# Optimization experiments

Hardware: AMD Instinct MI355X
Metric: run time of the kernel (lower is better)

The kernel has to match this reference:

```python
import jax, jax.numpy as jnp
import numpy as np

DIM = 1024
NUM_HEADS = 16
HEAD_DIM = DIM // NUM_HEADS
SCALE = HEAD_DIM ** -0.5


def rotate_half(x):
    x1, x2 = jnp.split(x, 2, axis=-1)
    return jnp.concatenate((-x2, x1), axis=-1)


def setup_inputs() -> dict:
    key = jax.random.key(0)
    ks = jax.random.split(key, 8)
    B, N = 2, 2048
    x = jax.random.normal(ks[0], (B, N, DIM), dtype=jnp.float32)
    # RoPE tables, broadcast over batch and heads
    pos = jnp.arange(N, dtype=jnp.float32)[:, None]
    inv_freq = 1.0 / (10000.0 ** (jnp.arange(0, HEAD_DIM, 2, dtype=jnp.float32) / HEAD_DIM))
    ang = pos * inv_freq[None, :]                       # [N, HEAD_DIM/2]
    ang = jnp.concatenate([ang, ang], axis=-1)          # [N, HEAD_DIM]
    rope_cos = jnp.cos(ang)[None, None]                 # [1,1,N,HEAD_DIM]
    rope_sin = jnp.sin(ang)[None, None]
    s = DIM ** -0.5
    qkv_w = jax.random.normal(ks[1], (3 * DIM, DIM), dtype=jnp.float32) * s
    qkv_b = jnp.zeros((3 * DIM,), dtype=jnp.float32)
    proj_w = jax.random.normal(ks[2], (DIM, DIM), dtype=jnp.float32) * s
    proj_b = jnp.zeros((DIM,), dtype=jnp.float32)
    return {"x": x, "rope_cos": rope_cos, "rope_sin": rope_sin,
            "qkv_w": qkv_w, "qkv_b": qkv_b, "proj_w": proj_w, "proj_b": proj_b}


def reference(x, rope_cos, rope_sin, qkv_w, qkv_b, proj_w, proj_b):
    B, N, C = x.shape
    H, D = NUM_HEADS, HEAD_DIM
    qkv = x @ qkv_w.T + qkv_b                            # [B,N,3C]
    qkv = qkv.reshape(B, N, 3, H, D).transpose(2, 0, 3, 1, 4)  # [3,B,H,N,D]
    q, k, v = qkv[0], qkv[1], qkv[2]
    # RoPE on q, k
    q = q * rope_cos + rotate_half(q) * rope_sin
    k = k * rope_cos + rotate_half(k) * rope_sin
    # scaled dot-product attention
    scores = jnp.einsum('bhnd,bhmd->bhnm', q, k) * SCALE
    attn = jax.nn.softmax(scores, axis=-1)
    out = jnp.einsum('bhnm,bhmd->bhnd', attn, v)         # [B,H,N,D]
    out = out.transpose(0, 2, 1, 3).reshape(B, N, C)
    return out @ proj_w.T + proj_b
```

## Files before the change

kernel.cpp:

```cpp
#include <hip/hip_runtime.h>
#include <hip/hip_bf16.h>

#define NUM_HEADS 16
#define HEAD_DIM 64
#define DIM 1024
#define NTOK 2048
#define MTOT 4096

typedef __attribute__((ext_vector_type(8))) short bf16x8;
typedef __attribute__((ext_vector_type(4))) float f32x4;

__device__ __forceinline__ unsigned short f2bf(float f) {
    union { __hip_bfloat16 h; unsigned short u; } c;
    c.h = __float2bfloat16(f);
    return c.u;
}

__device__ __forceinline__ void gload16(const unsigned short* g, unsigned short* l) {
    __builtin_amdgcn_global_load_lds(
        (const __attribute__((address_space(1))) void*)g,
        (__attribute__((address_space(3))) void*)l, 16, 0, 0);
}

__global__ __launch_bounds__(256) void k_conv3(
    const float* __restrict__ s0, unsigned short* __restrict__ d0, int n0,
    const float* __restrict__ s1, unsigned short* __restrict__ d1, int n1,
    const float* __restrict__ s2, unsigned short* __restrict__ d2, int n2)
{
    int blk = blockIdx.x;
    int b0 = n0 >> 11, b1 = n1 >> 11;
    const float* s; unsigned short* d; int i;
    if (blk < b0)            { s = s0; d = d0; i = blk; }
    else if (blk < b0 + b1)  { s = s1; d = d1; i = blk - b0; }
    else                     { s = s2; d = d2; i = blk - b0 - b1; }
    int idx = (i * 256 + threadIdx.x) * 8;
    float4 a = *(const float4*)(s + idx);
    float4 b = *(const float4*)(s + idx + 4);
    union { unsigned short us[8]; uint4 u4; } p;
    p.us[0] = f2bf(a.x); p.us[1] = f2bf(a.y); p.us[2] = f2bf(a.z); p.us[3] = f2bf(a.w);
    p.us[4] = f2bf(b.x); p.us[5] = f2bf(b.y); p.us[6] = f2bf(b.z); p.us[7] = f2bf(b.w);
    *(uint4*)(d + idx) = p.u4;
}

__global__ __launch_bounds__(256) void k_gemm_qkv(
    const unsigned short* __restrict__ xb, const unsigned short* __restrict__ wb,
    const float* __restrict__ bias, const float* __restrict__ rcos,
    const float* __restrict__ rsin,
    unsigned short* __restrict__ qb, unsigned short* __restrict__ kb,
    unsigned short* __restrict__ vtb)
{
    __shared__ __align__(16) unsigned char smem[34816];
    unsigned short* As = (unsigned short*)smem;
    unsigned short* Bs = (unsigned short*)(smem + 16384);

    const int tid  = threadIdx.x;
    const int lane = tid & 63;
    const int wid  = tid >> 6;
    const int lr   = lane & 15;
    const int g    = lane >> 4;
    const int wm   = (wid >> 1) * 64;
    const int wn   = (wid & 1) * 64;
    const int m0   = blockIdx.x * 128;
    const int n0   = blockIdx.y * 128;

    f32x4 acc[4][4];
    #pragma unroll
    for (int i = 0; i < 4; ++i)
        #pragma unroll
        for (int j = 0; j < 4; ++j) acc[i][j] = (f32x4){0.f, 0.f, 0.f, 0.f};

    for (int k0 = 0; k0 < DIM; k0 += 64) {
        #pragma unroll
        for (int it = 0; it < 4; ++it) {
            int p   = tid + it * 256;
            int row = p >> 3;
            int c   = (p & 7) ^ (row & 7);
            gload16(xb + (size_t)(m0 + row) * DIM + k0 + c*8, As + p*8);
            gload16(wb + (size_t)(n0 + row) * DIM + k0 + c*8, Bs + p*8);
        }
        __syncthreads();
        #pragma unroll
        for (int kk = 0; kk < 2; ++kk) {
            bf16x8 af[4], bfr[4];
            #pragma unroll
            for (int i = 0; i < 4; ++i) {
                int row = wm + i*16 + lr;
                af[i] = *(const bf16x8*)(As + row*64 + (((kk*4 + g) ^ (row & 7)) << 3));
            }
            #pragma unroll
            for (int j = 0; j < 4; ++j) {
                int row = wn + j*16 + lr;
                bfr[j] = *(const bf16x8*)(Bs + row*64 + (((kk*4 + g) ^ (row & 7)) << 3));
            }
            #pragma unroll
            for (int i = 0; i < 4; ++i)
                #pragma unroll
                for (int j = 0; j < 4; ++j)
                    acc[i][j] = __builtin_amdgcn_mfma_f32_16x16x32_bf16(af[i], bfr[j], acc[i][j], 0, 0, 0);
        }
        __syncthreads();
    }

    const int sect = n0 >> 10;
    float bq[4];
    #pragma unroll
    for (int j = 0; j < 4; ++j) bq[j] = bias[n0 + wn + j*16 + lr];

    if (sect < 2) {
        unsigned short* dst = sect ? kb : qb;
        const float sc = sect ? 1.0f : 0.125f * 1.44269504088896f;
        const int h = ((n0 & 1023) + wn) >> 6;
        #pragma unroll
        for (int i = 0; i < 4; ++i) {
            #pragma unroll
            for (int v = 0; v < 4; ++v) {
                int gm = m0 + wm + i*16 + g*4 + v;
                int b  = gm >> 11, n = gm & 2047;
                size_t base = ((size_t)(b*NUM_HEADS + h) * NTOK + n) << 6;
                #pragma unroll
                for (int j = 0; j < 4; ++j) {
                    int d = j*16 + lr;
                    float val = acc[i][j][v] + bq[j];
                    float vp  = acc[i][j^2][v] + bq[j^2];
                    float rot = (j < 2) ? -vp : vp;
                    float c = rcos[n*64 + d], s = rsin[n*64 + d];
                    dst[base + d] = f2bf((val * c + rot * s) * sc);
                }
            }
        }
    } else {
        unsigned short (*vt)[136] = (unsigned short (*)[136])smem;
        __syncthreads();
        #pragma unroll
        for (int i = 0; i < 4; ++i)
            #pragma unroll
            for (int j = 0; j < 4; ++j)
                #pragma unroll
                for (int v = 0; v < 4; ++v) {
                    int row = wm + i*16 + g*4 + v;
                    int c   = wn + j*16 + lr;
                    vt[c][row] = f2bf(acc[i][j][v] + bq[j]);
                }
        __syncthreads();
        const int b = m0 >> 11;
        const int nbase = m0 & 2047;
        #pragma unroll
        for (int it = 0; it < 8; ++it) {
            int c   = (tid >> 4) + it * 16;
            int sc2 = (n0 & 1023) + c;
            int hh  = sc2 >> 6, d = sc2 & 63;
            int nloc = (tid & 15) * 8;
            uint4 val = *(uint4*)&vt[c][nloc];
            *(uint4*)(vtb + ((size_t)(b*NUM_HEADS + hh) * HEAD_DIM + d) * NTOK + nbase + nloc) = val;
        }
    }
}

__global__ __launch_bounds__(256, 4) void k_attn(
    const unsigned short* __restrict__ qb, const unsigned short* __restrict__ kb,
    const unsigned short* __restrict__ vtb, unsigned short* __restrict__ attnb)
{
    __shared__ __align__(16) char sb[40960];

    const int tid  = threadIdx.x;
    const int lane = tid & 63;
    const int w    = tid >> 6;
    const int g    = lane >> 4;
    const int lr   = lane & 15;
    const int q0   = blockIdx.x * 64;
    const int bh   = blockIdx.y;
    const int b    = bh >> 4, h = bh & 15;

    int kfoff[2][4], vfoff[2][4];
    #pragma unroll
    for (int kk = 0; kk < 2; ++kk)
        #pragma unroll
        for (int fn = 0; fn < 4; ++fn) {
            int row = fn*16 + lr;
            int sw  = ((kk*4 + g) ^ (row & 7)) << 4;
            kfoff[kk][fn] = row*128 + sw;
            vfoff[kk][fn] = 16384 + row*128 + sw;
        }
    const int pswz = (lr & 7) << 1;
    int pwoff[4], proff[2];
    #pragma unroll
    for (int fn = 0; fn < 4; ++fn)
        pwoff[fn] = 32768 + w*2048 + lr*128 + (((fn*4 + g) ^ pswz) << 3);
    #pragma unroll
    for (int kk = 0; kk < 2; ++kk)
        proff[kk] = 32768 + w*2048 + lr*128 + (((kk*8 + g*2) ^ pswz) << 3);

    const unsigned short* gk[2];
    const unsigned short* gv[2];
    char* dk[2]; char* dv[2];
    {
        const unsigned short* kbase = kb  + (size_t)bh * NTOK * 64;
        const unsigned short* vbase = vtb + (size_t)bh * HEAD_DIM * NTOK;
        #pragma unroll
        for (int hp = 0; hp < 2; ++hp) {
            int p   = tid + hp * 256;
            int row = p >> 3;
            int c   = (p & 7) ^ (row & 7);
            gk[hp] = kbase + row*64 + c*8;
            gv[hp] = vbase + (size_t)row*NTOK + c*8;
            dk[hp] = sb + p*16;
            dv[hp] = sb + 16384 + p*16;
        }
    }

    bf16x8 qa[2];
    {
        size_t qrow = ((size_t)bh * NTOK + q0 + w*16 + lr) * 64;
        #pragma unroll
        for (int kk = 0; kk < 2; ++kk)
            qa[kk] = *(const bf16x8*)(qb + qrow + kk*32 + g*8);
    }

    const f32x4 z4 = {0.f, 0.f, 0.f, 0.f};
    bf16x8 onesa;
    #pragma unroll
    for (int j = 0; j < 8; ++j) onesa[j] = (short)0x3F80;

    f32x4 o2[4];
    f32x4 ol = z4;
    float m_ = -1e30f;
    #pragma unroll
    for (int fd = 0; fd < 4; ++fd) o2[fd] = z4;

    #pragma unroll
    for (int hp = 0; hp < 2; ++hp) {
        gload16(gk[hp], (unsigned short*)dk[hp]);
        gload16(gv[hp], (unsigned short*)dv[hp]);
        gk[hp] += 4096; gv[hp] += 64;
    }
    __syncthreads();

#define ATTN_ITER(X, DO_STAGE)                                                   \
    {                                                                            \
        if (DO_STAGE) {                                                          \
            _Pragma("unroll")                                                    \
            for (int hp = 0; hp < 2; ++hp) {                                     \
                gload16(gk[hp], (unsigned short*)(dk[hp] + ((X) ^ 8192)));       \
                gload16(gv[hp], (unsigned short*)(dv[hp] + ((X) ^ 8192)));       \
                gk[hp] += 4096; gv[hp] += 64;                                    \
            }                                                                    \
        }                                                                        \
        f32x4 s_[4];                                                             \
        __builtin_amdgcn_s_setprio(1);                                           \
        _Pragma("unroll")                                                        \
        for (int fn = 0; fn < 4; ++fn) {                                         \
            bf16x8 kf = *(const bf16x8*)(sb + kfoff[0][fn] + (X));               \
            s_[fn] = __builtin_amdgcn_mfma_f32_16x16x32_bf16(kf, qa[0], z4, 0, 0, 0); \
        }                                                                        \
        _Pragma("unroll")                                                        \
        for (int fn = 0; fn < 4; ++fn) {                                         \
            bf16x8 kf = *(const bf16x8*)(sb + kfoff[1][fn] + (X));               \
            s_[fn] = __builtin_amdgcn_mfma_f32_16x16x32_bf16(kf, qa[1], s_[fn], 0, 0, 0); \
        }                                                                        \
        __builtin_amdgcn_s_setprio(0);                                           \
        float mmA = fmaxf(fmaxf(s_[0][0], s_[0][1]), fmaxf(s_[0][2], s_[0][3])); \
        float mmB = fmaxf(fmaxf(s_[1][0], s_[1][1]), fmaxf(s_[1][2], s_[1][3])); \
        float mmC = fmaxf(fmaxf(s_[2][0], s_[2][1]), fmaxf(s_[2][2], s_[2][3])); \
        float mmD = fmaxf(fmaxf(s_[3][0], s_[3][1]), fmaxf(s_[3][2], s_[3][3])); \
        float lmax = fmaxf(fmaxf(mmA, mmB), fmaxf(mmC, mmD));                    \
        if (__any(lmax > m_ + 8.f)) {                                            \
            float mx = fmaxf(lmax, __shfl_xor(lmax, 16));                        \
            mx = fmaxf(mx, __shfl_xor(mx, 32));                                  \
            float mn  = fmaxf(m_, mx);                                           \
            float scl = __builtin_amdgcn_exp2f(m_ - mn);                         \
            m_ = mn;                                                             \
            _Pragma("unroll")                                                    \
            for (int v = 0; v < 4; ++v) ol[v] *= scl;                            \
            _Pragma("unroll")                                                    \
            for (int fd = 0; fd < 4; ++fd)                                       \
                _Pragma("unroll")                                                \
                for (int v = 0; v < 4; ++v) o2[fd][v] *= scl;                    \
        }                                                                        \
        _Pragma("unroll")                                                        \
        for (int fn = 0; fn < 4; ++fn) {                                         \
            union { unsigned short us[4]; uint2 u2; } pk4;                       \
            _Pragma("unroll")                                                    \
            for (int v = 0; v < 4; ++v)                                          \
                pk4.us[v] = f2bf(__builtin_amdgcn_exp2f(s_[fn][v] - m_));        \
            *(uint2*)(sb + pwoff[fn]) = pk4.u2;                                  \
        }                                                                        \
        _Pragma("unroll")                                                        \
        for (int kk = 0; kk < 2; ++kk) {                                         \
            bf16x8 pb = *(const bf16x8*)(sb + proff[kk]);                        \
            bf16x8 vf[4];                                                        \
            _Pragma("unroll")                                                    \
            for (int fd = 0; fd < 4; ++fd)                                       \
                vf[fd] = *(const bf16x8*)(sb + vfoff[kk][fd] + (X));             \
            __builtin_amdgcn_s_setprio(1);                                       \
            ol = __builtin_amdgcn_mfma_f32_16x16x32_bf16(onesa, pb, ol, 0, 0, 0); \
            _Pragma("unroll")                                                    \
            for (int fd = 0; fd < 4; ++fd)                                       \
                o2[fd] = __builtin_amdgcn_mfma_f32_16x16x32_bf16(vf[fd], pb, o2[fd], 0, 0, 0); \
            __builtin_amdgcn_s_setprio(0);                                       \
        }                                                                        \
        __syncthreads();                                                         \
    }

    #pragma unroll 1
    for (int t = 0; t < NTOK/64; t += 2) {
        ATTN_ITER(0,    true);
        ATTN_ITER(8192, (t + 2 < NTOK/64));
    }
#undef ATTN_ITER

    const float inv = 1.0f / ol[0];
    const size_t obase = ((size_t)(b*NTOK + q0 + w*16 + lr)) * DIM + h*HEAD_DIM + g*4;
    #pragma unroll
    for (int fd = 0; fd < 4; ++fd) {
        union { unsigned short us[4]; uint2 u2; } pk4;
        #pragma unroll
        for (int v = 0; v < 4; ++v) pk4.us[v] = f2bf(o2[fd][v] * inv);
        *(uint2*)(attnb + obase + fd*16) = pk4.u2;
    }
}

__global__ __launch_bounds__(256) void k_proj(
    const unsigned short* __restrict__ a, const unsigned short* __restrict__ wb,
    const float* __restrict__ bias, float* __restrict__ out)
{
    __shared__ __align__(16) unsigned short As[8192];
    __shared__ __align__(16) unsigned short Bs[8192];

    const int tid  = threadIdx.x;
    const int lane = tid & 63;
    const int wid  = tid >> 6;
    const int lr   = lane & 15;
    const int g    = lane >> 4;
    const int wm   = (wid >> 1) * 64;
    const int wn   = (wid & 1) * 64;
    const int m0   = blockIdx.x * 128;
    const int n0   = blockIdx.y * 128;

    f32x4 acc[4][4];
    #pragma unroll
    for (int i = 0; i < 4; ++i)
        #pragma unroll
        for (int j = 0; j < 4; ++j) acc[i][j] = (f32x4){0.f, 0.f, 0.f, 0.f};

    for (int k0 = 0; k0 < DIM; k0 += 64) {
        #pragma unroll
        for (int it = 0; it < 4; ++it) {
            int p   = tid + it * 256;
            int row = p >> 3;
            int c   = (p & 7) ^ (row & 7);
            gload16(a  + (size_t)(m0 + row) * DIM + k0 + c*8, As + p*8);
            gload16(wb + (size_t)(n0 + row) * DIM + k0 + c*8, Bs + p*8);
        }
        __syncthreads();
        #pragma unroll
        for (int kk = 0; kk < 2; ++kk) {
            bf16x8 af[4], bfr[4];
            #pragma unroll
            for (int i = 0; i < 4; ++i) {
                int row = wm + i*16 + lr;
                af[i] = *(const bf16x8*)(As + row*64 + (((kk*4 + g) ^ (row & 7)) << 3));
            }
            #pragma unroll
            for (int j = 0; j < 4; ++j) {
                int row = wn + j*16 + lr;
                bfr[j] = *(const bf16x8*)(Bs + row*64 + (((kk*4 + g) ^ (row & 7)) << 3));
            }
            #pragma unroll
            for (int i = 0; i < 4; ++i)
                #pragma unroll
                for (int j = 0; j < 4; ++j)
                    acc[i][j] = __builtin_amdgcn_mfma_f32_16x16x32_bf16(af[i], bfr[j], acc[i][j], 0, 0, 0);
        }
        __syncthreads();
    }

    #pragma unroll
    for (int i = 0; i < 4; ++i)
        #pragma unroll
        for (int j = 0; j < 4; ++j)
            #pragma unroll
            for (int v = 0; v < 4; ++v) {
                int row = m0 + wm + i*16 + g*4 + v;
                int col = n0 + wn + j*16 + lr;
                out[(size_t)row * DIM + col] = acc[i][j][v] + bias[col];
            }
}

extern "C" void kernel_launch(void* const* d_in, const int* in_sizes, int n_in,
                              void* d_out, int out_size, void* d_ws, size_t ws_size,
                              hipStream_t stream)
{
    const float* x      = (const float*)d_in[0];
    const float* rcos   = (const float*)d_in[1];
    const float* rsin   = (const float*)d_in[2];
    const float* qkv_w  = (const float*)d_in[3];
    const float* qkv_b  = (const float*)d_in[4];
    const float* proj_w = (const float*)d_in[5];
    const float* proj_b = (const float*)d_in[6];
    float* out = (float*)d_out;

    const size_t BUF = (size_t)2 * NUM_HEADS * NTOK * HEAD_DIM;
    unsigned short* qb    = (unsigned short*)d_ws;
    unsigned short* kb    = qb + BUF;
    unsigned short* vtb   = kb + BUF;
    unsigned short* attnb = vtb + BUF;
    unsigned short* xbf   = attnb + BUF;
    unsigned short* wqkvb = xbf + (size_t)MTOT * DIM;
    unsigned short* wprjb = wqkvb + (size_t)3 * DIM * DIM;

    const int n0 = MTOT * DIM, n1 = 3 * DIM * DIM, n2 = DIM * DIM;
    k_conv3<<<dim3((n0 + n1 + n2) / 2048), 256, 0, stream>>>(
        x, xbf, n0, qkv_w, wqkvb, n1, proj_w, wprjb, n2);

    k_gemm_qkv<<<dim3(32, 24), 256, 0, stream>>>(xbf, wqkvb, qkv_b, rcos, rsin, qb, kb, vtb);
    k_attn<<<dim3(NTOK/64, 32), 256, 0, stream>>>(qb, kb, vtb, attnb);
    k_proj<<<dim3(32, 8), 256, 0, stream>>>(attnb, wprjb, proj_b, out);
}
```

Baseline: 127.9 us.

## Use 32x32 MFMA with register-resident P in attention; retile projection GEMM

The attention kernel now uses 32x32x16 MFMA tiles with 128 queries per block. The probability matrix stays in registers, rearranged via permlane32 swaps instead of being written to and read back from LDS. The row sum is computed with VALU adds rather than an extra MFMA against a ones vector. The projection GEMM tile shrinks to 128x64, doubling the grid for better CU occupancy. The risks are more register pressure (launch bound lowered to 2 blocks/SM), half as many attention blocks, and extra VALU reduction work.

Result: faster. 121.5 us (-5.0%).

```diff
diff --git a/kernel.cpp b/kernel.cpp
--- a/kernel.cpp
+++ b/kernel.cpp
@@ -9,11 +9,33 @@
 
 typedef __attribute__((ext_vector_type(8))) short bf16x8;
 typedef __attribute__((ext_vector_type(4))) float f32x4;
+typedef __attribute__((ext_vector_type(16))) float f32x16;
+typedef __attribute__((ext_vector_type(2))) unsigned int uint2v;
 
 __device__ __forceinline__ unsigned short f2bf(float f) {
     union { __hip_bfloat16 h; unsigned short u; } c;
     c.h = __float2bfloat16(f);
     return c.u;
+}
+
+__device__ __forceinline__ unsigned int packbf(float lo, float hi) {
+    union { unsigned short us[2]; unsigned int u; } p;
+    p.us[0] = f2bf(lo); p.us[1] = f2bf(hi);
+    return p.u;
+}
+
+__device__ __forceinline__ void plswap(unsigned int &a, unsigned int &b) {
+#if __has_builtin(__builtin_amdgcn_permlane32_swap)
+    uint2v r = __builtin_amdgcn_permlane32_swap(a, b, false, false);
+    a = r[0]; b = r[1];
+#else
+    unsigned int pa = (unsigned int)__shfl_xor((int)a, 32);
+    unsigned int pb = (unsigned int)__shfl_xor((int)b, 32);
+    bool hi = (threadIdx.x & 32) != 0;
+    unsigned int an = hi ? pb : a;
+    unsigned int bn = hi ? b : pa;
+    a = an; b = bn;
+#endif
 }
 
 __device__ __forceinline__ void gload16(const unsigned short* g, unsigned short* l) {
@@ -156,39 +178,30 @@
     }
 }
 
-__global__ __launch_bounds__(256, 4) void k_attn(
+__global__ __launch_bounds__(256, 2) void k_attn(
     const unsigned short* __restrict__ qb, const unsigned short* __restrict__ kb,
     const unsigned short* __restrict__ vtb, unsigned short* __restrict__ attnb)
 {
-    __shared__ __align__(16) char sb[40960];
+    __shared__ __align__(16) char sb[32768];
 
     const int tid  = threadIdx.x;
     const int lane = tid & 63;
     const int w    = tid >> 6;
-    const int g    = lane >> 4;
-    const int lr   = lane & 15;
-    const int q0   = blockIdx.x * 64;
+    const int hi   = lane >> 5;
+    const int lc   = lane & 31;
+    const int q0   = blockIdx.x * 128;
     const int bh   = blockIdx.y;
     const int b    = bh >> 4, h = bh & 15;
 
     int kfoff[2][4], vfoff[2][4];
     #pragma unroll
-    for (int kk = 0; kk < 2; ++kk)
-        #pragma unroll
-        for (int fn = 0; fn < 4; ++fn) {
-            int row = fn*16 + lr;
-            int sw  = ((kk*4 + g) ^ (row & 7)) << 4;
-            kfoff[kk][fn] = row*128 + sw;
-            vfoff[kk][fn] = 16384 + row*128 + sw;
-        }
-    const int pswz = (lr & 7) << 1;
-    int pwoff[4], proff[2];
-    #pragma unroll
-    for (int fn = 0; fn < 4; ++fn)
-        pwoff[fn] = 32768 + w*2048 + lr*128 + (((fn*4 + g) ^ pswz) << 3);
-    #pragma unroll
-    for (int kk = 0; kk < 2; ++kk)
-        proff[kk] = 32768 + w*2048 + lr*128 + (((kk*8 + g*2) ^ pswz) << 3);
+    for (int s = 0; s < 2; ++s)
+        #pragma unroll
+        for (int ks = 0; ks < 4; ++ks) {
+            int row = 32*s + lc;
+            kfoff[s][ks] = row*128 + (((2*ks + hi) ^ (row & 7)) << 4);
+            vfoff[s][ks] = 16384 + row*128 + (((2*ks + hi) ^ (row & 7)) << 4);
+        }
 
     const unsigned short* gk[2];
     const unsigned short* gv[2];
@@ -208,24 +221,18 @@
         }
     }
 
-    bf16x8 qa[2];
+    bf16x8 qa[4];
     {
-        size_t qrow = ((size_t)bh * NTOK + q0 + w*16 + lr) * 64;
-        #pragma unroll
-        for (int kk = 0; kk < 2; ++kk)
-            qa[kk] = *(const bf16x8*)(qb + qrow + kk*32 + g*8);
-    }
-
-    const f32x4 z4 = {0.f, 0.f, 0.f, 0.f};
-    bf16x8 onesa;
-    #pragma unroll
-    for (int j = 0; j < 8; ++j) onesa[j] = (short)0x3F80;
-
-    f32x4 o2[4];
-    f32x4 ol = z4;
-    float m_ = -1e30f;
-    #pragma unroll
-    for (int fd = 0; fd < 4; ++fd) o2[fd] = z4;
+        size_t qrow = ((size_t)bh * NTOK + q0 + w*32 + lc) * 64;
+        #pragma unroll
+        for (int ks = 0; ks < 4; ++ks)
+            qa[ks] = *(const bf16x8*)(qb + qrow + ks*16 + hi*8);
+    }
+
+    const f32x16 z16 = {0.f,0.f,0.f,0.f, 0.f,0.f,0.f,0.f, 0.f,0.f,0.f,0.f, 0.f,0.f,0.f,0.f};
+    f32x16 o2[2];
+    o2[0] = z16; o2[1] = z16;
+    float m_ = -1e30f, lsum = 0.f;
 
     #pragma unroll
     for (int hp = 0; hp < 2; ++hp) {
@@ -245,78 +252,108 @@
                 gk[hp] += 4096; gv[hp] += 64;                                    \
             }                                                                    \
         }                                                                        \
-        f32x4 s_[4];                                                             \
-        __builtin_amdgcn_s_setprio(1);                                           \
-        _Pragma("unroll")                                                        \
-        for (int fn = 0; fn < 4; ++fn) {                                         \
-            bf16x8 kf = *(const bf16x8*)(sb + kfoff[0][fn] + (X));               \
-            s_[fn] = __builtin_amdgcn_mfma_f32_16x16x32_bf16(kf, qa[0], z4, 0, 0, 0); \
-        }                                                                        \
-        _Pragma("unroll")                                                        \
-        for (int fn = 0; fn < 4; ++fn) {                                         \
-            bf16x8 kf = *(const bf16x8*)(sb + kfoff[1][fn] + (X));               \
-            s_[fn] = __builtin_amdgcn_mfma_f32_16x16x32_bf16(kf, qa[1], s_[fn], 0, 0, 0); \
-        }                                                                        \
-        __builtin_amdgcn_s_setprio(0);                                           \
-        float mmA = fmaxf(fmaxf(s_[0][0], s_[0][1]), fmaxf(s_[0][2], s_[0][3])); \
-        float mmB = fmaxf(fmaxf(s_[1][0], s_[1][1]), fmaxf(s_[1][2], s_[1][3])); \
-        float mmC = fmaxf(fmaxf(s_[2][0], s_[2][1]), fmaxf(s_[2][2], s_[2][3])); \
-        float mmD = fmaxf(fmaxf(s_[3][0], s_[3][1]), fmaxf(s_[3][2], s_[3][3])); \
-        float lmax = fmaxf(fmaxf(mmA, mmB), fmaxf(mmC, mmD));                    \
+                                          \
+        f32x16 S0, S1;                                                           \
+        {                                                                        \
+            bf16x8 kf0[4], kf1[4];                                               \
+            _Pragma("unroll")                                                    \
+            for (int ks = 0; ks < 4; ++ks) {                                     \
+                kf0[ks] = *(const bf16x8*)(sb + kfoff[0][ks] + (X));             \
+                kf1[ks] = *(const bf16x8*)(sb + kfoff[1][ks] + (X));             \
+            }                                                                    \
+            __builtin_amdgcn_s_setprio(1);                                       \
+            S0 = __builtin_amdgcn_mfma_f32_32x32x16_bf16(kf0[0], qa[0], z16, 0, 0, 0); \
+            S1 = __builtin_amdgcn_mfma_f32_32x32x16_bf16(kf1[0], qa[0], z16, 0, 0, 0); \
+            _Pragma("unroll")                                                    \
+            for (int ks = 1; ks < 4; ++ks) {                                     \
+                S0 = __builtin_amdgcn_mfma_f32_32x32x16_bf16(kf0[ks], qa[ks], S0, 0, 0, 0); \
+                S1 = __builtin_amdgcn_mfma_f32_32x32x16_bf16(kf1[ks], qa[ks], S1, 0, 0, 0); \
+            }                                                                    \
+            __builtin_amdgcn_s_setprio(0);                                       \
+        }                                                                        \
+                          \
+        float t[16];                                                             \
+        _Pragma("unroll")                                                        \
+        for (int r = 0; r < 16; ++r) t[r] = fmaxf(S0[r], S1[r]);                 \
+        _Pragma("unroll")                                                        \
+        for (int st = 8; st > 0; st >>= 1)                                       \
+            _Pragma("unroll")                                                    \
+            for (int i = 0; i < 8; ++i) if (i < st) t[i] = fmaxf(t[i], t[i + st]); \
+        float lmax = t[0];                                                       \
         if (__any(lmax > m_ + 8.f)) {                                            \
-            float mx = fmaxf(lmax, __shfl_xor(lmax, 16));                        \
-            mx = fmaxf(mx, __shfl_xor(mx, 32));                                  \
-            float mn  = fmaxf(m_, mx);                                           \
+            float mx = fmaxf(lmax, __shfl_xor(lmax, 32));                        \
+            float mn = fmaxf(m_, mx);                                            \
             float scl = __builtin_amdgcn_exp2f(m_ - mn);                         \
             m_ = mn;                                                             \
+            lsum *= scl;                                                         \
+            o2[0] *= scl; o2[1] *= scl;                                          \
+        }                                                                        \
+                                               \
+        _Pragma("unroll")                                                        \
+        for (int r = 0; r < 16; ++r) {                                           \
+            S0[r] = __builtin_amdgcn_exp2f(S0[r] - m_);                          \
+            S1[r] = __builtin_amdgcn_exp2f(S1[r] - m_);                          \
+        }                                                                        \
+        _Pragma("unroll")                                                        \
+        for (int r = 0; r < 16; ++r) t[r] = S0[r] + S1[r];                       \
+        _Pragma("unroll")                                                        \
+        for (int st = 8; st > 0; st >>= 1)                                       \
             _Pragma("unroll")                                                    \
-            for (int v = 0; v < 4; ++v) ol[v] *= scl;                            \
-            _Pragma("unroll")                                                    \
-            for (int fd = 0; fd < 4; ++fd)                                       \
-                _Pragma("unroll")                                                \
-                for (int v = 0; v < 4; ++v) o2[fd][v] *= scl;                    \
-        }                                                                        \
-        _Pragma("unroll")                                                        \
-        for (int fn = 0; fn < 4; ++fn) {                                         \
-            union { unsigned short us[4]; uint2 u2; } pk4;                       \
-            _Pragma("unroll")                                                    \
-            for (int v = 0; v < 4; ++v)                                          \
-                pk4.us[v] = f2bf(__builtin_amdgcn_exp2f(s_[fn][v] - m_));        \
-            *(uint2*)(sb + pwoff[fn]) = pk4.u2;                                  \
-        }                                                                        \
-        _Pragma("unroll")                                                        \
-        for (int kk = 0; kk < 2; ++kk) {                                         \
-            bf16x8 pb = *(const bf16x8*)(sb + proff[kk]);                        \
-            bf16x8 vf[4];                                                        \
-            _Pragma("unroll")                                                    \
-            for (int fd = 0; fd < 4; ++fd)                                       \
-                vf[fd] = *(const bf16x8*)(sb + vfoff[kk][fd] + (X));             \
+            for (int i = 0; i < 8; ++i) if (i < st) t[i] += t[i + st];           \
+        lsum += t[0];                                                            \
+                \
+        unsigned int dwA[2][4], dwB[2][4];                                       \
+        _Pragma("unroll")                                                        \
+        for (int c = 0; c < 4; ++c) {                                            \
+            dwA[0][c] = packbf(S0[4*c],     S0[4*c + 1]);                        \
+            dwB[0][c] = packbf(S0[4*c + 2], S0[4*c + 3]);                        \
+            dwA[1][c] = packbf(S1[4*c],     S1[4*c + 1]);                        \
+            dwB[1][c] = packbf(S1[4*c + 2], S1[4*c + 3]);                        \
+        }                                                                        \
+        bf16x8 pB[4];                                                            \
+        _Pragma("unroll")                                                        \
+        for (int t16 = 0; t16 < 4; ++t16) {                                      \
+            int s = t16 >> 1, u = t16 & 1;                                       \
+            unsigned int a0 = dwA[s][2*u], b0 = dwA[s][2*u + 1];                 \
+            unsigned int a1 = dwB[s][2*u], b1 = dwB[s][2*u + 1];                 \
+            plswap(a0, b0);                                                      \
+            plswap(a1, b1);                                                      \
+            union { unsigned int u4[4]; bf16x8 v; } pk;                          \
+            pk.u4[0] = a0; pk.u4[1] = a1; pk.u4[2] = b0; pk.u4[3] = b1;          \
+            pB[t16] = pk.v;                                                      \
+        }                                                                        \
+                             \
+        _Pragma("unroll")                                                        \
+        for (int t16 = 0; t16 < 4; ++t16) {                                      \
+            bf16x8 vf0 = *(const bf16x8*)(sb + vfoff[0][t16] + (X));             \
+            bf16x8 vf1 = *(const bf16x8*)(sb + vfoff[1][t16] + (X));             \
             __builtin_amdgcn_s_setprio(1);                                       \
-            ol = __builtin_amdgcn_mfma_f32_16x16x32_bf16(onesa, pb, ol, 0, 0, 0); \
-            _Pragma("unroll")                                                    \
-            for (int fd = 0; fd < 4; ++fd)                                       \
-                o2[fd] = __builtin_amdgcn_mfma_f32_16x16x32_bf16(vf[fd], pb, o2[fd], 0, 0, 0); \
+            o2[0] = __builtin_amdgcn_mfma_f32_32x32x16_bf16(vf0, pB[t16], o2[0], 0, 0, 0); \
+            o2[1] = __builtin_amdgcn_mfma_f32_32x32x16_bf16(vf1, pB[t16], o2[1], 0, 0, 0); \
             __builtin_amdgcn_s_setprio(0);                                       \
         }                                                                        \
         __syncthreads();                                                         \
     }
 
     #pragma unroll 1
-    for (int t = 0; t < NTOK/64; t += 2) {
+    for (int tt = 0; tt < NTOK/64; tt += 2) {
         ATTN_ITER(0,    true);
-        ATTN_ITER(8192, (t + 2 < NTOK/64));
+        ATTN_ITER(8192, (tt + 2 < NTOK/64));
     }
 #undef ATTN_ITER
 
-    const float inv = 1.0f / ol[0];
-    const size_t obase = ((size_t)(b*NTOK + q0 + w*16 + lr)) * DIM + h*HEAD_DIM + g*4;
-    #pragma unroll
-    for (int fd = 0; fd < 4; ++fd) {
-        union { unsigned short us[4]; uint2 u2; } pk4;
-        #pragma unroll
-        for (int v = 0; v < 4; ++v) pk4.us[v] = f2bf(o2[fd][v] * inv);
-        *(uint2*)(attnb + obase + fd*16) = pk4.u2;
-    }
+    lsum += __shfl_xor(lsum, 32);
+    const float inv = 1.0f / lsum;
+    const size_t obase = ((size_t)(b*NTOK + q0 + w*32 + lc)) * DIM + h*HEAD_DIM + hi*4;
+    #pragma unroll
+    for (int sd = 0; sd < 2; ++sd)
+        #pragma unroll
+        for (int c = 0; c < 4; ++c) {
+            union { unsigned short us[4]; uint2 u2; } pk4;
+            #pragma unroll
+            for (int v = 0; v < 4; ++v) pk4.us[v] = f2bf(o2[sd][4*c + v] * inv);
+            *(uint2*)(attnb + obase + sd*32 + c*8) = pk4.u2;
+        }
 }
 
 __global__ __launch_bounds__(256) void k_proj(
@@ -324,23 +361,23 @@
     const float* __restrict__ bias, float* __restrict__ out)
 {
     __shared__ __align__(16) unsigned short As[8192];
-    __shared__ __align__(16) unsigned short Bs[8192];
+    __shared__ __align__(16) unsigned short Bs[4096];
 
     const int tid  = threadIdx.x;
     const int lane = tid & 63;
     const int wid  = tid >> 6;
     const int lr   = lane & 15;
     const int g    = lane >> 4;
-    const int wm   = (wid >> 1) * 64;
-    const int wn   = (wid & 1) * 64;
+    const int wm   = (wid & 1) * 64;
+    const int wn   = (wid >> 1) * 32;
     const int m0   = blockIdx.x * 128;
-    const int n0   = blockIdx.y * 128;
-
-    f32x4 acc[4][4];
+    const int n0   = blockIdx.y * 64;
+
+    f32x4 acc[4][2];
     #pragma unroll
     for (int i = 0; i < 4; ++i)
         #pragma unroll
-        for (int j = 0; j < 4; ++j) acc[i][j] = (f32x4){0.f, 0.f, 0.f, 0.f};
+        for (int j = 0; j < 2; ++j) acc[i][j] = (f32x4){0.f, 0.f, 0.f, 0.f};
 
     for (int k0 = 0; k0 < DIM; k0 += 64) {
         #pragma unroll
@@ -348,27 +385,33 @@
             int p   = tid + it * 256;
             int row = p >> 3;
             int c   = (p & 7) ^ (row & 7);
-            gload16(a  + (size_t)(m0 + row) * DIM + k0 + c*8, As + p*8);
+            gload16(a + (size_t)(m0 + row) * DIM + k0 + c*8, As + p*8);
+        }
+        #pragma unroll
+        for (int it = 0; it < 2; ++it) {
+            int p   = tid + it * 256;
+            int row = p >> 3;
+            int c   = (p & 7) ^ (row & 7);
             gload16(wb + (size_t)(n0 + row) * DIM + k0 + c*8, Bs + p*8);
         }
         __syncthreads();
         #pragma unroll
         for (int kk = 0; kk < 2; ++kk) {
-            bf16x8 af[4], bfr[4];
+            bf16x8 af[4], bfr[2];
             #pragma unroll
             for (int i = 0; i < 4; ++i) {
                 int row = wm + i*16 + lr;
                 af[i] = *(const bf16x8*)(As + row*64 + (((kk*4 + g) ^ (row & 7)) << 3));
             }
             #pragma unroll
-            for (int j = 0; j < 4; ++j) {
+            for (int j = 0; j < 2; ++j) {
                 int row = wn + j*16 + lr;
                 bfr[j] = *(const bf16x8*)(Bs + row*64 + (((kk*4 + g) ^ (row & 7)) << 3));
             }
             #pragma unroll
             for (int i = 0; i < 4; ++i)
                 #pragma unroll
-                for (int j = 0; j < 4; ++j)
+                for (int j = 0; j < 2; ++j)
                     acc[i][j] = __builtin_amdgcn_mfma_f32_16x16x32_bf16(af[i], bfr[j], acc[i][j], 0, 0, 0);
         }
         __syncthreads();
@@ -377,7 +420,7 @@
     #pragma unroll
     for (int i = 0; i < 4; ++i)
         #pragma unroll
-        for (int j = 0; j < 4; ++j)
+        for (int j = 0; j < 2; ++j)
             #pragma unroll
             for (int v = 0; v < 4; ++v) {
                 int row = m0 + wm + i*16 + g*4 + v;
@@ -413,6 +456,6 @@
         x, xbf, n0, qkv_w, wqkvb, n1, proj_w, wprjb, n2);
 
     k_gemm_qkv<<<dim3(32, 24), 256, 0, stream>>>(xbf, wqkvb, qkv_b, rcos, rsin, qb, kb, vtb);
-    k_attn<<<dim3(NTOK/64, 32), 256, 0, stream>>>(qb, kb, vtb, attnb);
-    k_proj<<<dim3(32, 8), 256, 0, stream>>>(attnb, wprjb, proj_b, out);
-}
+    k_attn<<<dim3(NTOK/128, 32), 256, 0, stream>>>(qb, kb, vtb, attnb);
+    k_proj<<<dim3(32, 16), 256, 0, stream>>>(attnb, wprjb, proj_b, out);
+}
```
